# Kernel optimization log

Hardware: AMD Instinct MI355X
Metric: run time of the kernel (lower is better)

## Reference

```python
import jax, jax.numpy as jnp
import numpy as np

B = 32; H = 56; W = 56; DIM = 192; WS = 7; SHIFT = 3; HEADS = 6
HEAD_DIM = DIM // HEADS; N = WS * WS; NW = (H // WS) * (W // WS)
HIDDEN = int(DIM * 4.0)
EPS = 1e-5


def _rel_pos_index():
    # standard Swin relative position index, shape (N, N), static
    coords = np.stack(np.meshgrid(np.arange(WS), np.arange(WS), indexing='ij'))  # (2, ws, ws)
    coords = coords.reshape(2, -1)                                               # (2, N)
    rel = (coords[:, :, None] - coords[:, None, :]).transpose(1, 2, 0)           # (N, N, 2)
    rel[:, :, 0] += WS - 1
    rel[:, :, 1] += WS - 1
    rel[:, :, 0] *= 2 * WS - 1
    return rel.sum(-1)  # (N, N)

REL_IDX = _rel_pos_index()


def _compute_attn_mask():
    # standard Swin SW-MSA mask, shape (NW, N, N), static
    img = np.zeros((H, W), dtype=np.float32)
    cnt = 0
    slices = (slice(0, -WS), slice(-WS, -SHIFT), slice(-SHIFT, None))
    for hs in slices:
        for ws_ in slices:
            img[hs, ws_] = cnt
            cnt += 1
    mw = img.reshape(H // WS, WS, W // WS, WS).transpose(0, 2, 1, 3).reshape(-1, N)  # (NW, N)
    diff = mw[:, None, :] - mw[:, :, None]
    return np.where(diff != 0, np.float32(-100.0), np.float32(0.0))


def _layernorm(x, g, b):
    mu = jnp.mean(x, axis=-1, keepdims=True)
    var = jnp.mean(jnp.square(x - mu), axis=-1, keepdims=True)
    return (x - mu) * jax.lax.rsqrt(var + EPS) * g + b


def setup_inputs() -> dict:
    key = jax.random.key(0)
    ks = jax.random.split(key, 8)
    s = 0.02
    inp = {
        'x': jax.random.normal(ks[0], (B, H * W, DIM), dtype=jnp.float32),
        'g1': jnp.ones((DIM,), jnp.float32), 'b1': jnp.zeros((DIM,), jnp.float32),
        'qkv_w': jax.random.normal(ks[1], (DIM, 3 * DIM), jnp.float32) * s,
        'qkv_b': jnp.zeros((3 * DIM,), jnp.float32),
        'proj_w': jax.random.normal(ks[2], (DIM, DIM), jnp.float32) * s,
        'proj_b': jnp.zeros((DIM,), jnp.float32),
        'rel_table': jax.random.normal(ks[3], ((2 * WS - 1) ** 2, HEADS), jnp.float32) * s,
        'g2': jnp.ones((DIM,), jnp.float32), 'b2': jnp.zeros((DIM,), jnp.float32),
        'fc1_w': jax.random.normal(ks[4], (DIM, HIDDEN), jnp.float32) * s,
        'fc1_b': jnp.zeros((HIDDEN,), jnp.float32),
        'fc2_w': jax.random.normal(ks[5], (HIDDEN, DIM), jnp.float32) * s,
        'fc2_b': jnp.zeros((DIM,), jnp.float32),
        'attn_mask': jnp.asarray(_compute_attn_mask()),
    }
    return inp


def reference(x, g1, b1, qkv_w, qkv_b, proj_w, proj_b, rel_table, g2, b2,
              fc1_w, fc1_b, fc2_w, fc2_b, attn_mask):
    shortcut = x
    h = _layernorm(x, g1, b1).reshape(B, H, W, DIM)
    h = jnp.roll(h, (-SHIFT, -SHIFT), axis=(1, 2))
    # window partition -> (B*NW, N, C)
    win = h.reshape(B, H // WS, WS, W // WS, WS, DIM).transpose(0, 1, 3, 2, 4, 5)
    win = win.reshape(-1, N, DIM)
    qkv = (win @ qkv_w + qkv_b).reshape(-1, N, 3, HEADS, HEAD_DIM).transpose(2, 0, 3, 1, 4)
    q, k, v = qkv[0], qkv[1], qkv[2]                         # (B*NW, heads, N, d)
    attn = jnp.einsum('whnd,whmd->whnm', q, k) * (HEAD_DIM ** -0.5)
    bias = rel_table[REL_IDX.reshape(-1)].reshape(N, N, HEADS).transpose(2, 0, 1)
    attn = attn + bias[None]
    attn = attn.reshape(B, NW, HEADS, N, N) + attn_mask[None, :, None]
    attn = jax.nn.softmax(attn, axis=-1).reshape(-1, HEADS, N, N)
    out = jnp.einsum('whnm,whmd->whnd', attn, v).transpose(0, 2, 1, 3).reshape(-1, N, DIM)
    out = out @ proj_w + proj_b
    # window reverse -> (B, H, W, C)
    out = out.reshape(B, H // WS, W // WS, WS, WS, DIM).transpose(0, 1, 3, 2, 4, 5)
    out = out.reshape(B, H, W, DIM)
    out = jnp.roll(out, (SHIFT, SHIFT), axis=(1, 2)).reshape(B, H * W, DIM)
    x = shortcut + out
    shortcut2 = x
    h = _layernorm(x, g2, b2)
    h = jax.nn.gelu(h @ fc1_w + fc1_b, approximate=False)
    h = h @ fc2_w + fc2_b
    return shortcut2 + h
```

## Files before the change

### kernel.cpp

```cpp
#include <hip/hip_runtime.h>
#include <math.h>

#define B_      32
#define HH      56
#define WW_     56
#define DIM     192
#define WS_     7
#define SHIFT_  3
#define HEADS   6
#define HDIM    32
#define NTOK    49
#define NWIN    64
#define HIDDEN  768
#define MTOT    (B_*HH*WW_)
#define EPS_    1e-5f
#define SCALE_  0.17677669529663687f

#define ALD 200
#define PLD 40
#define VLD 72

#define MROWS 64
#define HLDQ  200

typedef unsigned short u16;
typedef __attribute__((ext_vector_type(8))) __bf16 bf16x8;
typedef __attribute__((ext_vector_type(4))) float f32x4;

__device__ __forceinline__ float bf2f(u16 u) {
    union { unsigned int i; float f; } c; c.i = ((unsigned int)u) << 16; return c.f;
}
__device__ __forceinline__ u16 f2bf(float f) {
    union { float f; unsigned int i; } c; c.f = f;
    unsigned int x = c.i;
    return (u16)((x + 0x7FFFu + ((x >> 16) & 1u)) >> 16);
}

__device__ __forceinline__ float wave_sum(float v) {
    #pragma unroll
    for (int off = 32; off > 0; off >>= 1) v += __shfl_xor(v, off, 64);
    return v;
}

__global__ __launch_bounds__(256) void prep_kernel(
        const float* __restrict__ qkv_w, const float* __restrict__ proj_w,
        const float* __restrict__ fc1_w, const float* __restrict__ fc2_w,
        u16* __restrict__ qkv_wT, u16* __restrict__ proj_wT,
        u16* __restrict__ fc1_wT, u16* __restrict__ fc2_wT,
        const float* __restrict__ rel_table, const float* __restrict__ mask,
        float* __restrict__ tbl) {
    __shared__ float t[32][33];
    int b = blockIdx.x;
    const float* W; u16* Wt; int K, N, tb;
    if (b < 108)      { W = qkv_w;  Wt = qkv_wT;  K = DIM;    N = 3 * DIM; tb = b; }
    else if (b < 144) { W = proj_w; Wt = proj_wT; K = DIM;    N = DIM;     tb = b - 108; }
    else if (b < 288) { W = fc1_w;  Wt = fc1_wT;  K = DIM;    N = HIDDEN;  tb = b - 144; }
    else if (b < 432) { W = fc2_w;  Wt = fc2_wT;  K = HIDDEN; N = DIM;     tb = b - 288; }
    else {
        int idx = (b - 432) * 256 + threadIdx.x;
        int kj   = idx & 63;
        int qi   = (idx >> 6) & 63;
        int head = (idx >> 12) % 6;
        int wl   = idx / (6 << 12);
        float v;
        if (qi < NTOK && kj < NTOK) {
            int qr = qi / WS_, qc = qi % WS_;
            int kr = kj / WS_, kc = kj % WS_;
            int ri = (qr - kr + 6) * 13 + (qc - kc + 6);
            v = rel_table[ri * HEADS + head] + mask[((size_t)wl * NTOK + qi) * NTOK + kj];
        } else {
            v = -1e30f;
        }
        tbl[idx] = v;
        return;
    }
    int nt32 = N >> 5;
    int bx = tb % nt32;
    int by = tb / nt32;
    int tx = threadIdx.x & 31, ty = threadIdx.x >> 5;
    #pragma unroll
    for (int i = 0; i < 4; i++)
        t[ty + i * 8][tx] = W[(size_t)(by * 32 + ty + i * 8) * N + bx * 32 + tx];
    __syncthreads();
    #pragma unroll
    for (int i = 0; i < 4; i++)
        Wt[(size_t)(bx * 32 + ty + i * 8) * K + by * 32 + tx] = f2bf(t[tx][ty + i * 8]);
}

__global__ __launch_bounds__(256) void ln1_window_kernel(
        const float* __restrict__ x, const float* __restrict__ g,
        const float* __restrict__ b, u16* __restrict__ out) {
    int row  = blockIdx.x * 4 + (threadIdx.x >> 6);
    int lane = threadIdx.x & 63;
    int win = row / NTOK;
    int n   = row - win * NTOK;
    int bb  = win >> 6;
    int wl  = win & 63;
    int hi  = (wl >> 3) * WS_ + n / WS_;
    int hj  = (wl & 7) * WS_ + n % WS_;
    int sh = hi + SHIFT_; if (sh >= HH) sh -= HH;
    int sw = hj + SHIFT_; if (sw >= WW_) sw -= WW_;
    const float* xr = x + ((size_t)(bb * HH * WW_ + sh * WW_ + sw)) * DIM;
    float v0 = xr[lane], v1 = xr[lane + 64], v2 = xr[lane + 128];
    float s  = wave_sum(v0 + v1 + v2);
    float sq = wave_sum(v0 * v0 + v1 * v1 + v2 * v2);
    float mu  = s * (1.0f / DIM);
    float var = sq * (1.0f / DIM) - mu * mu;
    float r = rsqrtf(var + EPS_);
    u16* orow = out + (size_t)row * DIM;
    orow[lane]       = f2bf((v0 - mu) * r * g[lane]       + b[lane]);
    orow[lane + 64]  = f2bf((v1 - mu) * r * g[lane + 64]  + b[lane + 64]);
    orow[lane + 128] = f2bf((v2 - mu) * r * g[lane + 128] + b[lane + 128]);
}

__global__ __launch_bounds__(256) void ln2_kernel(
        const float* __restrict__ x, const float* __restrict__ g,
        const float* __restrict__ b, u16* __restrict__ out) {
    int row  = blockIdx.x * 4 + (threadIdx.x >> 6);
    int lane = threadIdx.x & 63;
    const float* xr = x + (size_t)row * DIM;
    float v0 = xr[lane], v1 = xr[lane + 64], v2 = xr[lane + 128];
    float s  = wave_sum(v0 + v1 + v2);
    float sq = wave_sum(v0 * v0 + v1 * v1 + v2 * v2);
    float mu  = s * (1.0f / DIM);
    float var = sq * (1.0f / DIM) - mu * mu;
    float r = rsqrtf(var + EPS_);
    u16* orow = out + (size_t)row * DIM;
    orow[lane]       = f2bf((v0 - mu) * r * g[lane]       + b[lane]);
    orow[lane + 64]  = f2bf((v1 - mu) * r * g[lane + 64]  + b[lane + 64]);
    orow[lane + 128] = f2bf((v2 - mu) * r * g[lane + 128] + b[lane + 128]);
}

__global__ __launch_bounds__(384) void fused_attn_kernel(
        const u16* __restrict__ hwin, const u16* __restrict__ qkv_wT,
        const float* __restrict__ qkv_b, const u16* __restrict__ proj_wT,
        const float* __restrict__ proj_b, const float* __restrict__ tbl,
        const float* __restrict__ x, float* __restrict__ x1) {
    __shared__ u16 sm[29184];
    u16* R1 = sm;
    u16* Vt = sm + 15360;

    const int tid  = threadIdx.x;
    const int w    = tid >> 6;
    const int lane = tid & 63;
    const int lrow = lane & 15, lq = lane >> 4;
    const int win  = blockIdx.x;
    const int wl   = win & 63, bb = win >> 6;

    {
        const uint4* src = (const uint4*)(hwin + (size_t)win * NTOK * DIM);
        uint4 z; z.x = z.y = z.z = z.w = 0u;
        #pragma unroll
        for (int it = 0; it < 4; it++) {
            int i = tid + it * 384;
            int row = i / 24, c = i - row * 24;
            uint4 v = (row < NTOK) ? src[row * 24 + c] : z;
            *(uint4*)&R1[row * ALD + c * 8] = v;
        }
    }
    __syncthreads();

    f32x4 acc[3][4][2];
    #pragma unroll
    for (int o = 0; o < 3; o++)
        #pragma unroll
        for (int mt = 0; mt < 4; mt++)
            #pragma unroll
            for (int nt = 0; nt < 2; nt++) acc[o][mt][nt] = (f32x4){0.f, 0.f, 0.f, 0.f};

    const u16* bcol[3][2];
    #pragma unroll
    for (int o = 0; o < 3; o++)
        #pragma unroll
        for (int nt = 0; nt < 2; nt++)
            bcol[o][nt] = qkv_wT + (size_t)(o * DIM + w * 32 + nt * 16 + lrow) * DIM + lq * 8;

    #pragma unroll
    for (int ks = 0; ks < 6; ks++) {
        bf16x8 aF[4];
        #pragma unroll
        for (int mt = 0; mt < 4; mt++)
            aF[mt] = *(const bf16x8*)&R1[(mt * 16 + lrow) * ALD + ks * 32 + lq * 8];
        bf16x8 bF[3][2];
        #pragma unroll
        for (int o = 0; o < 3; o++)
            #pragma unroll
            for (int nt = 0; nt < 2; nt++)
                bF[o][nt] = *(const bf16x8*)(bcol[o][nt] + ks * 32);
        __builtin_amdgcn_s_setprio(1);
        #pragma unroll
        for (int o = 0; o < 3; o++)
            #pragma unroll
            for (int mt = 0; mt < 4; mt++)
                #pragma unroll
                for (int nt = 0; nt < 2; nt++)
                    acc[o][mt][nt] = __builtin_amdgcn_mfma_f32_16x16x32_bf16(
                        aF[mt], bF[o][nt], acc[o][mt][nt], 0, 0, 0);
        __builtin_amdgcn_s_setprio(0);
    }
    float bias_[3][2];
    #pragma unroll
    for (int o = 0; o < 3; o++)
        #pragma unroll
        for (int nt = 0; nt < 2; nt++)
            bias_[o][nt] = qkv_b[o * DIM + w * 32 + nt * 16 + lrow];
    #pragma unroll
    for (int o = 0; o < 3; o++)
        #pragma unroll
        for (int mt = 0; mt < 4; mt++)
            #pragma unroll
            for (int nt = 0; nt < 2; nt++)
                #pragma unroll
                for (int r = 0; r < 4; r++) acc[o][mt][nt][r] += bias_[o][nt];

    __syncthreads();

    #pragma unroll
    for (int mt = 0; mt < 4; mt++)
        #pragma unroll
        for (int nt = 0; nt < 2; nt++)
            #pragma unroll
            for (int r = 0; r < 4; r++)
                R1[(mt * 16 + lq * 4 + r) * ALD + w * 32 + nt * 16 + lrow] =
                    f2bf(acc[0][mt][nt][r]);
    bf16x8 qf[4];
    #pragma unroll
    for (int mt = 0; mt < 4; mt++)
        qf[mt] = *(const bf16x8*)&R1[(mt * 16 + lrow) * ALD + w * 32 + lq * 8];

    #pragma unroll
    for (int mt = 0; mt < 4; mt++)
        #pragma unroll
        for (int nt = 0; nt < 2; nt++)
            #pragma unroll
            for (int r = 0; r < 4; r++)
                R1[(mt * 16 + lq * 4 + r) * ALD + w * 32 + nt * 16 + lrow] =
                    f2bf(acc[1][mt][nt][r]);
    bf16x8 kf[4];
    #pragma unroll
    for (int nt = 0; nt < 4; nt++)
        kf[nt] = *(const bf16x8*)&R1[(nt * 16 + lrow) * ALD + w * 32 + lq * 8];

    #pragma unroll
    for (int mt = 0; mt < 4; mt++)
        #pragma unroll
        for (int nt = 0; nt < 2; nt++)
            #pragma unroll
            for (int r = 0; r < 4; r++)
                Vt[(w * 32 + nt * 16 + lrow) * VLD + mt * 16 + lq * 4 + r] =
                    f2bf(acc[2][mt][nt][r]);

    f32x4 sc[4][4];
    __builtin_amdgcn_s_setprio(1);
    #pragma unroll
    for (int mt = 0; mt < 4; mt++)
        #pragma unroll
        for (int nt = 0; nt < 4; nt++) {
            f32x4 z = (f32x4){0.f, 0.f, 0.f, 0.f};
            sc[mt][nt] = __builtin_amdgcn_mfma_f32_16x16x32_bf16(qf[mt], kf[nt], z, 0, 0, 0);
        }
    __builtin_amdgcn_s_setprio(0);
    const float* tb = tbl + (((size_t)wl * HEADS + w) << 12);
    float inv[4][4];
    #pragma unroll
    for (int mt = 0; mt < 4; mt++)
        #pragma unroll
        for (int r = 0; r < 4; r++) {
            int qi = mt * 16 + lq * 4 + r;
            float mx = -3.0e38f;
            #pragma unroll
            for (int nt = 0; nt < 4; nt++) {
                float s = sc[mt][nt][r] * SCALE_ + tb[(qi << 6) + nt * 16 + lrow];
                sc[mt][nt][r] = s;
                mx = fmaxf(mx, s);
            }
            #pragma unroll
            for (int off = 8; off > 0; off >>= 1) mx = fmaxf(mx, __shfl_xor(mx, off, 64));
            float sum = 0.f;
            #pragma unroll
            for (int nt = 0; nt < 4; nt++) {
                float e = __expf(sc[mt][nt][r] - mx);
                sc[mt][nt][r] = e;
                sum += e;
            }
            #pragma unroll
            for (int off = 8; off > 0; off >>= 1) sum += __shfl_xor(sum, off, 64);
            inv[mt][r] = 1.0f / sum;
        }

    u16* Pl = R1 + w * (64 * PLD);
    f32x4 oc[4][2];
    #pragma unroll
    for (int mt = 0; mt < 4; mt++)
        #pragma unroll
        for (int nd = 0; nd < 2; nd++) oc[mt][nd] = (f32x4){0.f, 0.f, 0.f, 0.f};
    #pragma unroll
    for (int ks = 0; ks < 2; ks++) {
        #pragma unroll
        for (int mt = 0; mt < 4; mt++)
            #pragma unroll
            for (int ntl = 0; ntl < 2; ntl++)
                #pragma unroll
                for (int r = 0; r < 4; r++)
                    Pl[(mt * 16 + lq * 4 + r) * PLD + ntl * 16 + lrow] =
                        f2bf(sc[mt][ks * 2 + ntl][r]);
        bf16x8 vf[2];
        #pragma unroll
        for (int nd = 0; nd < 2; nd++)
            vf[nd] = *(const bf16x8*)&Vt[(w * 32 + nd * 16 + lrow) * VLD + ks * 32 + lq * 8];
        __builtin_amdgcn_s_setprio(1);
        #pragma unroll
        for (int mt = 0; mt < 4; mt++) {
            bf16x8 pf = *(const bf16x8*)&Pl[(mt * 16 + lrow) * PLD + lq * 8];
            #pragma unroll
            for (int nd = 0; nd < 2; nd++)
                oc[mt][nd] = __builtin_amdgcn_mfma_f32_16x16x32_bf16(pf, vf[nd],
                                                                     oc[mt][nd], 0, 0, 0);
        }
        __builtin_amdgcn_s_setprio(0);
    }
    __syncthreads();

    #pragma unroll
    for (int mt = 0; mt < 4; mt++)
        #pragma unroll
        for (int nd = 0; nd < 2; nd++)
            #pragma unroll
            for (int r = 0; r < 4; r++)
                R1[(mt * 16 + lq * 4 + r) * ALD + w * 32 + nd * 16 + lrow] =
                    f2bf(oc[mt][nd][r] * inv[mt][r]);
    __syncthreads();

    f32x4 pacc[4][2];
    #pragma unroll
    for (int mt = 0; mt < 4; mt++)
        #pragma unroll
        for (int nt = 0; nt < 2; nt++) pacc[mt][nt] = (f32x4){0.f, 0.f, 0.f, 0.f};
    const u16* pcol[2];
    #pragma unroll
    for (int nt = 0; nt < 2; nt++)
        pcol[nt] = proj_wT + (size_t)(w * 32 + nt * 16 + lrow) * DIM + lq * 8;
    #pragma unroll
    for (int ks = 0; ks < 6; ks++) {
        bf16x8 af[4];
        #pragma unroll
        for (int mt = 0; mt < 4; mt++)
            af[mt] = *(const bf16x8*)&R1[(mt * 16 + lrow) * ALD + ks * 32 + lq * 8];
        bf16x8 pb[2];
        #pragma unroll
        for (int nt = 0; nt < 2; nt++) pb[nt] = *(const bf16x8*)(pcol[nt] + ks * 32);
        __builtin_amdgcn_s_setprio(1);
        #pragma unroll
        for (int mt = 0; mt < 4; mt++)
            #pragma unroll
            for (int nt = 0; nt < 2; nt++)
                pacc[mt][nt] = __builtin_amdgcn_mfma_f32_16x16x32_bf16(
                    af[mt], pb[nt], pacc[mt][nt], 0, 0, 0);
        __builtin_amdgcn_s_setprio(0);
    }
    float pbias[2];
    #pragma unroll
    for (int nt = 0; nt < 2; nt++) pbias[nt] = proj_b[w * 32 + nt * 16 + lrow];
    #pragma unroll
    for (int mt = 0; mt < 4; mt++)
        #pragma unroll
        for (int r = 0; r < 4; r++) {
            int n = mt * 16 + lq * 4 + r;
            if (n < NTOK) {
                int hi = (wl >> 3) * WS_ + n / WS_;
                int hj = (wl & 7) * WS_ + n % WS_;
                int dh = hi + SHIFT_; if (dh >= HH) dh -= HH;
                int dw = hj + SHIFT_; if (dw >= WW_) dw -= WW_;
                size_t tok = (size_t)(bb * HH * WW_ + dh * WW_ + dw);
                #pragma unroll
                for (int nt = 0; nt < 2; nt++) {
                    int col = w * 32 + nt * 16 + lrow;
                    x1[tok * DIM + col] = x[tok * DIM + col] + pacc[mt][nt][r] + pbias[nt];
                }
            }
        }
}

__global__ __launch_bounds__(384) void mlp_fused_kernel(
        const u16* __restrict__ h2, const u16* __restrict__ fc1_wT,
        const float* __restrict__ fc1_b, const u16* __restrict__ fc2_wT,
        const float* __restrict__ fc2_b, float* __restrict__ out) {
    __shared__ u16 Ash[MROWS * ALD];
    __shared__ u16 Hsh[MROWS * HLDQ];

    const int tid  = threadIdx.x;
    const int w    = tid >> 6;
    const int lane = tid & 63;
    const int lrow = lane & 15, lq = lane >> 4;
    const int m0   = blockIdx.x * MROWS;

    {
        const uint4* src = (const uint4*)(h2 + (size_t)m0 * DIM);
        #pragma unroll
        for (int it = 0; it < 4; it++) {
            int i = tid + it * 384;
            int row = i / 24, c = i - row * 24;
            *(uint4*)&Ash[row * ALD + c * 8] = src[row * 24 + c];
        }
    }
    __syncthreads();

    f32x4 acc2[4][2];
    #pragma unroll
    for (int mt = 0; mt < 4; mt++)
        #pragma unroll
        for (int nt = 0; nt < 2; nt++) acc2[mt][nt] = (f32x4){0.f, 0.f, 0.f, 0.f};

    for (int h = 0; h < 4; h++) {
        f32x4 hacc[4][2];
        #pragma unroll
        for (int mt = 0; mt < 4; mt++)
            #pragma unroll
            for (int nt = 0; nt < 2; nt++) hacc[mt][nt] = (f32x4){0.f, 0.f, 0.f, 0.f};
        const u16* b1base = fc1_wT + (size_t)(h * 192 + w * 32) * DIM;
        #pragma unroll
        for (int ks = 0; ks < 6; ks++) {
            bf16x8 aF[4];
            #pragma unroll
            for (int mt = 0; mt < 4; mt++)
                aF[mt] = *(const bf16x8*)&Ash[(mt * 16 + lrow) * ALD + ks * 32 + lq * 8];
            bf16x8 bF[2];
            #pragma unroll
            for (int nt = 0; nt < 2; nt++)
                bF[nt] = *(const bf16x8*)(b1base + (size_t)(nt * 16 + lrow) * DIM +
                                          ks * 32 + lq * 8);
            __builtin_amdgcn_s_setprio(1);
            #pragma unroll
            for (int mt = 0; mt < 4; mt++)
                #pragma unroll
                for (int nt = 0; nt < 2; nt++)
                    hacc[mt][nt] = __builtin_amdgcn_mfma_f32_16x16x32_bf16(
                        aF[mt], bF[nt], hacc[mt][nt], 0, 0, 0);
            __builtin_amdgcn_s_setprio(0);
        }
        if (h) __syncthreads();
        #pragma unroll
        for (int nt = 0; nt < 2; nt++) {
            float bv = fc1_b[h * 192 + w * 32 + nt * 16 + lrow];
            #pragma unroll
            for (int mt = 0; mt < 4; mt++)
                #pragma unroll
                for (int r = 0; r < 4; r++) {
                    float val = hacc[mt][nt][r] + bv;
                    float gel = 0.5f * val * (1.0f + erff(val * 0.70710678118f));
                    Hsh[(mt * 16 + lq * 4 + r) * HLDQ + w * 32 + nt * 16 + lrow] = f2bf(gel);
                }
        }
        __syncthreads();

        const u16* b2base = fc2_wT + (size_t)(w * 32) * HIDDEN + h * 192;
        #pragma unroll
        for (int ks = 0; ks < 6; ks++) {
            bf16x8 hF[4];
            #pragma unroll
            for (int mt = 0; mt < 4; mt++)
                hF[mt] = *(const bf16x8*)&Hsh[(mt * 16 + lrow) * HLDQ + ks * 32 + lq * 8];
            bf16x8 b2F[2];
            #pragma unroll
            for (int nt = 0; nt < 2; nt++)
                b2F[nt] = *(const bf16x8*)(b2base + (size_t)(nt * 16 + lrow) * HIDDEN +
                                           ks * 32 + lq * 8);
            __builtin_amdgcn_s_setprio(1);
            #pragma unroll
            for (int mt = 0; mt < 4; mt++)
                #pragma unroll
                for (int nt = 0; nt < 2; nt++)
                    acc2[mt][nt] = __builtin_amdgcn_mfma_f32_16x16x32_bf16(
                        hF[mt], b2F[nt], acc2[mt][nt], 0, 0, 0);
            __builtin_amdgcn_s_setprio(0);
        }
    }

    #pragma unroll
    for (int nt = 0; nt < 2; nt++) {
        int col = w * 32 + nt * 16 + lrow;
        float bv = fc2_b[col];
        #pragma unroll
        for (int mt = 0; mt < 4; mt++)
            #pragma unroll
            for (int r = 0; r < 4; r++) {
                size_t grow = (size_t)(m0 + mt * 16 + lq * 4 + r);
                out[grow * DIM + col] = out[grow * DIM + col] + acc2[mt][nt][r] + bv;
            }
    }
}

extern "C" void kernel_launch(void* const* d_in, const int* in_sizes, int n_in,
                              void* d_out, int out_size, void* d_ws, size_t ws_size,
                              hipStream_t stream) {
    const float* x         = (const float*)d_in[0];
    const float* g1        = (const float*)d_in[1];
    const float* b1        = (const float*)d_in[2];
    const float* qkv_w     = (const float*)d_in[3];
    const float* qkv_b     = (const float*)d_in[4];
    const float* proj_w    = (const float*)d_in[5];
    const float* proj_b    = (const float*)d_in[6];
    const float* rel_table = (const float*)d_in[7];
    const float* g2        = (const float*)d_in[8];
    const float* b2        = (const float*)d_in[9];
    const float* fc1_w     = (const float*)d_in[10];
    const float* fc1_b     = (const float*)d_in[11];
    const float* fc2_w     = (const float*)d_in[12];
    const float* fc2_b     = (const float*)d_in[13];
    const float* attn_mask = (const float*)d_in[14];
    float* out = (float*)d_out;

    const size_t S = (size_t)MTOT * DIM;
    u16* wsu = (u16*)d_ws;
    u16*   hwin    = wsu;
    u16*   wT      = wsu + S;
    u16*   qkv_wT  = wT;
    u16*   proj_wT = wT + 110592;
    u16*   fc1_wT  = wT + 147456;
    u16*   fc2_wT  = wT + 294912;
    float* tbl     = (float*)(wT + 442368);

    prep_kernel<<<432 + (NWIN * HEADS * 64 * 64) / 256, 256, 0, stream>>>(
        qkv_w, proj_w, fc1_w, fc2_w, qkv_wT, proj_wT, fc1_wT, fc2_wT,
        rel_table, attn_mask, tbl);

    ln1_window_kernel<<<MTOT / 4, 256, 0, stream>>>(x, g1, b1, hwin);
    fused_attn_kernel<<<B_ * NWIN, 384, 0, stream>>>(hwin, qkv_wT, qkv_b, proj_wT, proj_b,
                                                     tbl, x, out);
    ln2_kernel<<<MTOT / 4, 256, 0, stream>>>(out, g2, b2, hwin);
    mlp_fused_kernel<<<MTOT / MROWS, 384, 0, stream>>>(hwin, fc1_wT, fc1_b, fc2_wT, fc2_b, out);
}
```

Before: 493.5 us.

## Merge LN1 into prep kernel and software-pipeline fc1/fc2 chunks in MLP

```diff
diff --git a/kernel.cpp b/kernel.cpp
--- a/kernel.cpp
+++ b/kernel.cpp
@@ -48,15 +48,36 @@
         u16* __restrict__ qkv_wT, u16* __restrict__ proj_wT,
         u16* __restrict__ fc1_wT, u16* __restrict__ fc2_wT,
         const float* __restrict__ rel_table, const float* __restrict__ mask,
-        float* __restrict__ tbl) {
+        float* __restrict__ tbl,
+        const float* __restrict__ x, const float* __restrict__ g1,
+        const float* __restrict__ b1, u16* __restrict__ hwin) {
     __shared__ float t[32][33];
     int b = blockIdx.x;
-    const float* W; u16* Wt; int K, N, tb;
-    if (b < 108)      { W = qkv_w;  Wt = qkv_wT;  K = DIM;    N = 3 * DIM; tb = b; }
-    else if (b < 144) { W = proj_w; Wt = proj_wT; K = DIM;    N = DIM;     tb = b - 108; }
-    else if (b < 288) { W = fc1_w;  Wt = fc1_wT;  K = DIM;    N = HIDDEN;  tb = b - 144; }
-    else if (b < 432) { W = fc2_w;  Wt = fc2_wT;  K = HIDDEN; N = DIM;     tb = b - 288; }
-    else {
+    if (b >= 6576) {
+        int row  = (b - 6576) * 4 + (threadIdx.x >> 6);
+        int lane = threadIdx.x & 63;
+        int win = row / NTOK;
+        int n   = row - win * NTOK;
+        int bb  = win >> 6;
+        int wl  = win & 63;
+        int hi  = (wl >> 3) * WS_ + n / WS_;
+        int hj  = (wl & 7) * WS_ + n % WS_;
+        int sh = hi + SHIFT_; if (sh >= HH) sh -= HH;
+        int sw = hj + SHIFT_; if (sw >= WW_) sw -= WW_;
+        const float* xr = x + ((size_t)(bb * HH * WW_ + sh * WW_ + sw)) * DIM;
+        float v0 = xr[lane], v1 = xr[lane + 64], v2 = xr[lane + 128];
+        float s  = wave_sum(v0 + v1 + v2);
+        float sq = wave_sum(v0 * v0 + v1 * v1 + v2 * v2);
+        float mu  = s * (1.0f / DIM);
+        float var = sq * (1.0f / DIM) - mu * mu;
+        float r = rsqrtf(var + EPS_);
+        u16* orow = hwin + (size_t)row * DIM;
+        orow[lane]       = f2bf((v0 - mu) * r * g1[lane]       + b1[lane]);
+        orow[lane + 64]  = f2bf((v1 - mu) * r * g1[lane + 64]  + b1[lane + 64]);
+        orow[lane + 128] = f2bf((v2 - mu) * r * g1[lane + 128] + b1[lane + 128]);
+        return;
+    }
+    if (b >= 432) {
         int idx = (b - 432) * 256 + threadIdx.x;
         int kj   = idx & 63;
         int qi   = (idx >> 6) & 63;
@@ -74,6 +95,11 @@
         tbl[idx] = v;
         return;
     }
+    const float* W; u16* Wt; int K, N, tb;
+    if (b < 108)      { W = qkv_w;  Wt = qkv_wT;  K = DIM;    N = 3 * DIM; tb = b; }
+    else if (b < 144) { W = proj_w; Wt = proj_wT; K = DIM;    N = DIM;     tb = b - 108; }
+    else if (b < 288) { W = fc1_w;  Wt = fc1_wT;  K = DIM;    N = HIDDEN;  tb = b - 144; }
+    else              { W = fc2_w;  Wt = fc2_wT;  K = HIDDEN; N = DIM;     tb = b - 288; }
     int nt32 = N >> 5;
     int bx = tb % nt32;
     int by = tb / nt32;
@@ -85,32 +111,6 @@
     #pragma unroll
     for (int i = 0; i < 4; i++)
         Wt[(size_t)(bx * 32 + ty + i * 8) * K + by * 32 + tx] = f2bf(t[tx][ty + i * 8]);
-}
-
-__global__ __launch_bounds__(256) void ln1_window_kernel(
-        const float* __restrict__ x, const float* __restrict__ g,
-        const float* __restrict__ b, u16* __restrict__ out) {
-    int row  = blockIdx.x * 4 + (threadIdx.x >> 6);
-    int lane = threadIdx.x & 63;
-    int win = row / NTOK;
-    int n   = row - win * NTOK;
-    int bb  = win >> 6;
-    int wl  = win & 63;
-    int hi  = (wl >> 3) * WS_ + n / WS_;
-    int hj  = (wl & 7) * WS_ + n % WS_;
-    int sh = hi + SHIFT_; if (sh >= HH) sh -= HH;
-    int sw = hj + SHIFT_; if (sw >= WW_) sw -= WW_;
-    const float* xr = x + ((size_t)(bb * HH * WW_ + sh * WW_ + sw)) * DIM;
-    float v0 = xr[lane], v1 = xr[lane + 64], v2 = xr[lane + 128];
-    float s  = wave_sum(v0 + v1 + v2);
-    float sq = wave_sum(v0 * v0 + v1 * v1 + v2 * v2);
-    float mu  = s * (1.0f / DIM);
-    float var = sq * (1.0f / DIM) - mu * mu;
-    float r = rsqrtf(var + EPS_);
-    u16* orow = out + (size_t)row * DIM;
-    orow[lane]       = f2bf((v0 - mu) * r * g[lane]       + b[lane]);
-    orow[lane + 64]  = f2bf((v1 - mu) * r * g[lane + 64]  + b[lane + 64]);
-    orow[lane + 128] = f2bf((v2 - mu) * r * g[lane + 128] + b[lane + 128]);
 }
 
 __global__ __launch_bounds__(256) void ln2_kernel(
@@ -406,18 +406,17 @@
     __syncthreads();
 
     f32x4 acc2[4][2];
-    #pragma unroll
-    for (int mt = 0; mt < 4; mt++)
-        #pragma unroll
-        for (int nt = 0; nt < 2; nt++) acc2[mt][nt] = (f32x4){0.f, 0.f, 0.f, 0.f};
-
-    for (int h = 0; h < 4; h++) {
-        f32x4 hacc[4][2];
-        #pragma unroll
-        for (int mt = 0; mt < 4; mt++)
-            #pragma unroll
-            for (int nt = 0; nt < 2; nt++) hacc[mt][nt] = (f32x4){0.f, 0.f, 0.f, 0.f};
-        const u16* b1base = fc1_wT + (size_t)(h * 192 + w * 32) * DIM;
+    f32x4 hacc[4][2];
+    #pragma unroll
+    for (int mt = 0; mt < 4; mt++)
+        #pragma unroll
+        for (int nt = 0; nt < 2; nt++) {
+            acc2[mt][nt] = (f32x4){0.f, 0.f, 0.f, 0.f};
+            hacc[mt][nt] = (f32x4){0.f, 0.f, 0.f, 0.f};
+        }
+
+    {
+        const u16* b1base = fc1_wT + (size_t)(w * 32) * DIM;
         #pragma unroll
         for (int ks = 0; ks < 6; ks++) {
             bf16x8 aF[4];
@@ -438,10 +437,9 @@
                         aF[mt], bF[nt], hacc[mt][nt], 0, 0, 0);
             __builtin_amdgcn_s_setprio(0);
         }
-        if (h) __syncthreads();
         #pragma unroll
         for (int nt = 0; nt < 2; nt++) {
-            float bv = fc1_b[h * 192 + w * 32 + nt * 16 + lrow];
+            float bv = fc1_b[w * 32 + nt * 16 + lrow];
             #pragma unroll
             for (int mt = 0; mt < 4; mt++)
                 #pragma unroll
@@ -451,8 +449,18 @@
                     Hsh[(mt * 16 + lq * 4 + r) * HLDQ + w * 32 + nt * 16 + lrow] = f2bf(gel);
                 }
         }
-        __syncthreads();
-
+    }
+    __syncthreads();
+
+    #pragma unroll
+    for (int h = 0; h < 4; h++) {
+        if (h < 3) {
+            #pragma unroll
+            for (int mt = 0; mt < 4; mt++)
+                #pragma unroll
+                for (int nt = 0; nt < 2; nt++) hacc[mt][nt] = (f32x4){0.f, 0.f, 0.f, 0.f};
+        }
+        const u16* b1base = fc1_wT + (size_t)((h + 1) * 192 + w * 32) * DIM;
         const u16* b2base = fc2_wT + (size_t)(w * 32) * HIDDEN + h * 192;
         #pragma unroll
         for (int ks = 0; ks < 6; ks++) {
@@ -465,6 +473,16 @@
             for (int nt = 0; nt < 2; nt++)
                 b2F[nt] = *(const bf16x8*)(b2base + (size_t)(nt * 16 + lrow) * HIDDEN +
                                            ks * 32 + lq * 8);
+            bf16x8 aF[4], bF[2];
+            if (h < 3) {
+                #pragma unroll
+                for (int mt = 0; mt < 4; mt++)
+                    aF[mt] = *(const bf16x8*)&Ash[(mt * 16 + lrow) * ALD + ks * 32 + lq * 8];
+                #pragma unroll
+                for (int nt = 0; nt < 2; nt++)
+                    bF[nt] = *(const bf16x8*)(b1base + (size_t)(nt * 16 + lrow) * DIM +
+                                              ks * 32 + lq * 8);
+            }
             __builtin_amdgcn_s_setprio(1);
             #pragma unroll
             for (int mt = 0; mt < 4; mt++)
@@ -472,7 +490,32 @@
                 for (int nt = 0; nt < 2; nt++)
                     acc2[mt][nt] = __builtin_amdgcn_mfma_f32_16x16x32_bf16(
                         hF[mt], b2F[nt], acc2[mt][nt], 0, 0, 0);
+            if (h < 3) {
+                #pragma unroll
+                for (int mt = 0; mt < 4; mt++)
+                    #pragma unroll
+                    for (int nt = 0; nt < 2; nt++)
+                        hacc[mt][nt] = __builtin_amdgcn_mfma_f32_16x16x32_bf16(
+                            aF[mt], bF[nt], hacc[mt][nt], 0, 0, 0);
+            }
             __builtin_amdgcn_s_setprio(0);
+        }
+        __syncthreads();
+        if (h < 3) {
+            #pragma unroll
+            for (int nt = 0; nt < 2; nt++) {
+                float bv = fc1_b[(h + 1) * 192 + w * 32 + nt * 16 + lrow];
+                #pragma unroll
+                for (int mt = 0; mt < 4; mt++)
+                    #pragma unroll
+                    for (int r = 0; r < 4; r++) {
+                        float val = hacc[mt][nt][r] + bv;
+                        float gel = 0.5f * val * (1.0f + erff(val * 0.70710678118f));
+                        Hsh[(mt * 16 + lq * 4 + r) * HLDQ + w * 32 + nt * 16 + lrow] =
+                            f2bf(gel);
+                    }
+            }
+            __syncthreads();
         }
     }
 
@@ -520,11 +563,10 @@
     u16*   fc2_wT  = wT + 294912;
     float* tbl     = (float*)(wT + 442368);
 
-    prep_kernel<<<432 + (NWIN * HEADS * 64 * 64) / 256, 256, 0, stream>>>(
+    prep_kernel<<<432 + (NWIN * HEADS * 64 * 64) / 256 + MTOT / 4, 256, 0, stream>>>(
         qkv_w, proj_w, fc1_w, fc2_w, qkv_wT, proj_wT, fc1_wT, fc2_wT,
-        rel_table, attn_mask, tbl);
-
-    ln1_window_kernel<<<MTOT / 4, 256, 0, stream>>>(x, g1, b1, hwin);
+        rel_table, attn_mask, tbl, x, g1, b1, hwin);
+
     fused_attn_kernel<<<B_ * NWIN, 384, 0, stream>>>(hwin, qkv_wT, qkv_b, proj_wT, proj_b,
                                                      tbl, x, out);
     ln2_kernel<<<MTOT / 4, 256, 0, stream>>>(out, g2, b2, hwin);
```

Result: slower. 578.2 us (+17.2%).

## Fuse LayerNorm1 into prep kernel and LayerNorm2 into MLP prologue

Applied to the files above, without the earlier changes.

```diff
diff --git a/kernel.cpp b/kernel.cpp
--- a/kernel.cpp
+++ b/kernel.cpp
@@ -48,15 +48,36 @@
         u16* __restrict__ qkv_wT, u16* __restrict__ proj_wT,
         u16* __restrict__ fc1_wT, u16* __restrict__ fc2_wT,
         const float* __restrict__ rel_table, const float* __restrict__ mask,
-        float* __restrict__ tbl) {
+        float* __restrict__ tbl,
+        const float* __restrict__ x, const float* __restrict__ g1,
+        const float* __restrict__ b1, u16* __restrict__ hwin) {
     __shared__ float t[32][33];
     int b = blockIdx.x;
-    const float* W; u16* Wt; int K, N, tb;
-    if (b < 108)      { W = qkv_w;  Wt = qkv_wT;  K = DIM;    N = 3 * DIM; tb = b; }
-    else if (b < 144) { W = proj_w; Wt = proj_wT; K = DIM;    N = DIM;     tb = b - 108; }
-    else if (b < 288) { W = fc1_w;  Wt = fc1_wT;  K = DIM;    N = HIDDEN;  tb = b - 144; }
-    else if (b < 432) { W = fc2_w;  Wt = fc2_wT;  K = HIDDEN; N = DIM;     tb = b - 288; }
-    else {
+    if (b >= 6576) {
+        int row  = (b - 6576) * 4 + (threadIdx.x >> 6);
+        int lane = threadIdx.x & 63;
+        int win = row / NTOK;
+        int n   = row - win * NTOK;
+        int bb  = win >> 6;
+        int wl  = win & 63;
+        int hi  = (wl >> 3) * WS_ + n / WS_;
+        int hj  = (wl & 7) * WS_ + n % WS_;
+        int sh = hi + SHIFT_; if (sh >= HH) sh -= HH;
+        int sw = hj + SHIFT_; if (sw >= WW_) sw -= WW_;
+        const float* xr = x + ((size_t)(bb * HH * WW_ + sh * WW_ + sw)) * DIM;
+        float v0 = xr[lane], v1 = xr[lane + 64], v2 = xr[lane + 128];
+        float s  = wave_sum(v0 + v1 + v2);
+        float sq = wave_sum(v0 * v0 + v1 * v1 + v2 * v2);
+        float mu  = s * (1.0f / DIM);
+        float var = sq * (1.0f / DIM) - mu * mu;
+        float r = rsqrtf(var + EPS_);
+        u16* orow = hwin + (size_t)row * DIM;
+        orow[lane]       = f2bf((v0 - mu) * r * g1[lane]       + b1[lane]);
+        orow[lane + 64]  = f2bf((v1 - mu) * r * g1[lane + 64]  + b1[lane + 64]);
+        orow[lane + 128] = f2bf((v2 - mu) * r * g1[lane + 128] + b1[lane + 128]);
+        return;
+    }
+    if (b >= 432) {
         int idx = (b - 432) * 256 + threadIdx.x;
         int kj   = idx & 63;
         int qi   = (idx >> 6) & 63;
@@ -74,6 +95,11 @@
         tbl[idx] = v;
         return;
     }
+    const float* W; u16* Wt; int K, N, tb;
+    if (b < 108)      { W = qkv_w;  Wt = qkv_wT;  K = DIM;    N = 3 * DIM; tb = b; }
+    else if (b < 144) { W = proj_w; Wt = proj_wT; K = DIM;    N = DIM;     tb = b - 108; }
+    else if (b < 288) { W = fc1_w;  Wt = fc1_wT;  K = DIM;    N = HIDDEN;  tb = b - 144; }
+    else              { W = fc2_w;  Wt = fc2_wT;  K = HIDDEN; N = DIM;     tb = b - 288; }
     int nt32 = N >> 5;
     int bx = tb % nt32;
     int by = tb / nt32;
@@ -85,50 +111,6 @@
     #pragma unroll
     for (int i = 0; i < 4; i++)
         Wt[(size_t)(bx * 32 + ty + i * 8) * K + by * 32 + tx] = f2bf(t[tx][ty + i * 8]);
-}
-
-__global__ __launch_bounds__(256) void ln1_window_kernel(
-        const float* __restrict__ x, const float* __restrict__ g,
-        const float* __restrict__ b, u16* __restrict__ out) {
-    int row  = blockIdx.x * 4 + (threadIdx.x >> 6);
-    int lane = threadIdx.x & 63;
-    int win = row / NTOK;
-    int n   = row - win * NTOK;
-    int bb  = win >> 6;
-    int wl  = win & 63;
-    int hi  = (wl >> 3) * WS_ + n / WS_;
-    int hj  = (wl & 7) * WS_ + n % WS_;
-    int sh = hi + SHIFT_; if (sh >= HH) sh -= HH;
-    int sw = hj + SHIFT_; if (sw >= WW_) sw -= WW_;
-    const float* xr = x + ((size_t)(bb * HH * WW_ + sh * WW_ + sw)) * DIM;
-    float v0 = xr[lane], v1 = xr[lane + 64], v2 = xr[lane + 128];
-    float s  = wave_sum(v0 + v1 + v2);
-    float sq = wave_sum(v0 * v0 + v1 * v1 + v2 * v2);
-    float mu  = s * (1.0f / DIM);
-    float var = sq * (1.0f / DIM) - mu * mu;
-    float r = rsqrtf(var + EPS_);
-    u16* orow = out + (size_t)row * DIM;
-    orow[lane]       = f2bf((v0 - mu) * r * g[lane]       + b[lane]);
-    orow[lane + 64]  = f2bf((v1 - mu) * r * g[lane + 64]  + b[lane + 64]);
-    orow[lane + 128] = f2bf((v2 - mu) * r * g[lane + 128] + b[lane + 128]);
-}
-
-__global__ __launch_bounds__(256) void ln2_kernel(
-        const float* __restrict__ x, const float* __restrict__ g,
-        const float* __restrict__ b, u16* __restrict__ out) {
-    int row  = blockIdx.x * 4 + (threadIdx.x >> 6);
-    int lane = threadIdx.x & 63;
-    const float* xr = x + (size_t)row * DIM;
-    float v0 = xr[lane], v1 = xr[lane + 64], v2 = xr[lane + 128];
-    float s  = wave_sum(v0 + v1 + v2);
-    float sq = wave_sum(v0 * v0 + v1 * v1 + v2 * v2);
-    float mu  = s * (1.0f / DIM);
-    float var = sq * (1.0f / DIM) - mu * mu;
-    float r = rsqrtf(var + EPS_);
-    u16* orow = out + (size_t)row * DIM;
-    orow[lane]       = f2bf((v0 - mu) * r * g[lane]       + b[lane]);
-    orow[lane + 64]  = f2bf((v1 - mu) * r * g[lane + 64]  + b[lane + 64]);
-    orow[lane + 128] = f2bf((v2 - mu) * r * g[lane + 128] + b[lane + 128]);
 }
 
 __global__ __launch_bounds__(384) void fused_attn_kernel(
@@ -382,9 +364,10 @@
 }
 
 __global__ __launch_bounds__(384) void mlp_fused_kernel(
-        const u16* __restrict__ h2, const u16* __restrict__ fc1_wT,
-        const float* __restrict__ fc1_b, const u16* __restrict__ fc2_wT,
-        const float* __restrict__ fc2_b, float* __restrict__ out) {
+        const float* __restrict__ g2, const float* __restrict__ b2,
+        const u16* __restrict__ fc1_wT, const float* __restrict__ fc1_b,
+        const u16* __restrict__ fc2_wT, const float* __restrict__ fc2_b,
+        float* __restrict__ out) {
     __shared__ u16 Ash[MROWS * ALD];
     __shared__ u16 Hsh[MROWS * HLDQ];
 
@@ -395,12 +378,35 @@
     const int m0   = blockIdx.x * MROWS;
 
     {
-        const uint4* src = (const uint4*)(h2 + (size_t)m0 * DIM);
-        #pragma unroll
-        for (int it = 0; it < 4; it++) {
-            int i = tid + it * 384;
-            int row = i / 24, c = i - row * 24;
-            *(uint4*)&Ash[row * ALD + c * 8] = src[row * 24 + c];
+        float gA = g2[lane], gB = g2[lane + 64], gC = g2[lane + 128];
+        float bA = b2[lane], bB = b2[lane + 64], bC = b2[lane + 128];
+        const float* xrow = out + (size_t)m0 * DIM;
+        float va[11][3];
+        #pragma unroll
+        for (int k = 0; k < 11; k++) {
+            int r = w + 6 * k;
+            if (r < MROWS) {
+                const float* xr = xrow + (size_t)r * DIM;
+                va[k][0] = xr[lane];
+                va[k][1] = xr[lane + 64];
+                va[k][2] = xr[lane + 128];
+            }
+        }
+        #pragma unroll
+        for (int k = 0; k < 11; k++) {
+            int r = w + 6 * k;
+            if (r < MROWS) {
+                float s  = wave_sum(va[k][0] + va[k][1] + va[k][2]);
+                float sq = wave_sum(va[k][0] * va[k][0] + va[k][1] * va[k][1] +
+                                    va[k][2] * va[k][2]);
+                float mu  = s * (1.0f / DIM);
+                float var = sq * (1.0f / DIM) - mu * mu;
+                float rr  = rsqrtf(var + EPS_);
+                u16* arow = &Ash[r * ALD];
+                arow[lane]       = f2bf((va[k][0] - mu) * rr * gA + bA);
+                arow[lane + 64]  = f2bf((va[k][1] - mu) * rr * gB + bB);
+                arow[lane + 128] = f2bf((va[k][2] - mu) * rr * gC + bC);
+            }
         }
     }
     __syncthreads();
@@ -520,13 +526,12 @@
     u16*   fc2_wT  = wT + 294912;
     float* tbl     = (float*)(wT + 442368);
 
-    prep_kernel<<<432 + (NWIN * HEADS * 64 * 64) / 256, 256, 0, stream>>>(
+    prep_kernel<<<432 + (NWIN * HEADS * 64 * 64) / 256 + MTOT / 4, 256, 0, stream>>>(
         qkv_w, proj_w, fc1_w, fc2_w, qkv_wT, proj_wT, fc1_wT, fc2_wT,
-        rel_table, attn_mask, tbl);
-
-    ln1_window_kernel<<<MTOT / 4, 256, 0, stream>>>(x, g1, b1, hwin);
+        rel_table, attn_mask, tbl, x, g1, b1, hwin);
+
     fused_attn_kernel<<<B_ * NWIN, 384, 0, stream>>>(hwin, qkv_wT, qkv_b, proj_wT, proj_b,
                                                      tbl, x, out);
-    ln2_kernel<<<MTOT / 4, 256, 0, stream>>>(out, g2, b2, hwin);
-    mlp_fused_kernel<<<MTOT / MROWS, 384, 0, stream>>>(hwin, fc1_wT, fc1_b, fc2_wT, fc2_b, out);
-}
+    mlp_fused_kernel<<<MTOT / MROWS, 384, 0, stream>>>(g2, b2, fc1_wT, fc1_b,
+                                                       fc2_wT, fc2_b, out);
+}
```

After: 477.6 us. 3.2% less time.
